# Kernel tuning notes

Hardware: AMD Instinct MI355X
Metric: run time of the kernel (lower is better)

Reference implementation:

```python
import jax, jax.numpy as jnp
import numpy as np

D_MODEL, D_LOW, NUM_BINS = 512, 64, 39
DIST_MIN, DIST_MAX = 2.0, 22.0
BIN_WIDTH = (DIST_MAX - DIST_MIN) / (NUM_BINS - 1)
LN_EPS = 1e-5


def setup_inputs() -> dict:
    key = jax.random.key(0)
    ks = jax.random.split(key, 10)
    B, N = 2, 768
    h_res = jax.random.normal(ks[0], (B, N, D_MODEL), dtype=jnp.float32)
    # scale coords so pairwise distances span the [2, 22] bin range
    x_true = jax.random.normal(ks[1], (B, N, 3), dtype=jnp.float32) * 5.0
    token_pad_mask = jnp.ones((B, N), dtype=jnp.float32)
    s = 1.0 / np.sqrt(D_MODEL)
    return {
        "h_res": h_res,
        "x_true": x_true,
        "token_pad_mask": token_pad_mask,
        "ln_w": jnp.ones((D_MODEL,), jnp.float32),
        "ln_b": jnp.zeros((D_MODEL,), jnp.float32),
        "wu_w": jax.random.normal(ks[2], (D_LOW, D_MODEL), jnp.float32) * s,
        "wu_b": jnp.zeros((D_LOW,), jnp.float32),
        "wv_w": jax.random.normal(ks[3], (D_LOW, D_MODEL), jnp.float32) * s,
        "wv_b": jnp.zeros((D_LOW,), jnp.float32),
        "wb_w": jax.random.normal(ks[4], (NUM_BINS, D_LOW), jnp.float32) * (1.0 / np.sqrt(D_LOW)),
        "wb_b": jnp.zeros((NUM_BINS,), jnp.float32),
    }


def _layernorm(x, w, b):
    mu = jnp.mean(x, axis=-1, keepdims=True)
    var = jnp.mean(jnp.square(x - mu), axis=-1, keepdims=True)
    return (x - mu) * jax.lax.rsqrt(var + LN_EPS) * w + b


def reference(h_res, x_true, token_pad_mask, ln_w, ln_b, wu_w, wu_b, wv_w, wv_b, wb_w, wb_b):
    B, N, _ = h_res.shape
    # pairwise distances -> target bins (trunc-to-int then clamp, as torch .long())
    diff = x_true[:, :, None, :] - x_true[:, None, :, :]          # [B,N,N,3]
    d_true = jnp.sqrt(jnp.sum(diff * diff, axis=-1))               # [B,N,N]
    target = jnp.clip(((d_true - DIST_MIN) / BIN_WIDTH).astype(jnp.int32), 0, NUM_BINS - 1)

    h = _layernorm(h_res, ln_w, ln_b)
    U = h @ wu_w.T + wu_b                                          # [B,N,d_low]
    V = h @ wv_w.T + wv_b                                          # [B,N,d_low]
    # logits[b,i,j,k] = sum_c U[b,i,c] V[b,j,c] Wb[k,c] + bb[k]
    logits = jnp.einsum("bic,bjc,kc->bijk", U, V, wb_w) + wb_b     # [B,N,N,K]
    logp = jax.nn.log_softmax(logits, axis=-1)
    ce = -jnp.take_along_axis(logp, target[..., None], axis=-1)[..., 0]  # [B,N,N]

    mask = (token_pad_mask[:, :, None] * token_pad_mask[:, None, :]) > 0  # [B,N,N] bool
    counts = jnp.sum(mask, axis=(1, 2))                            # [B]
    per_sample = jnp.sum(jnp.where(mask, ce, 0.0), axis=(1, 2)) / jnp.maximum(counts, 1)
    valid = counts > 0
    total_count = jnp.sum(valid)
    loss = jnp.sum(jnp.where(valid, per_sample, 0.0)) / jnp.maximum(total_count, 1)
    return loss
```

## Files before the change

kernel.cpp:

```cpp
#include <hip/hip_runtime.h>
#include <hip/hip_bf16.h>
#include <math.h>

#define D_MODEL 512
#define D_LOW   64
#define NBINS   39
#define LOG2E   1.4426950408889634f
#define LN2     0.6931471805599453f

typedef __attribute__((ext_vector_type(8))) short short8;
typedef __attribute__((ext_vector_type(4))) float floatx4;

__global__ __launch_bounds__(256) void prep_kernel(
    const float* __restrict__ ln_w, const float* __restrict__ ln_b,
    const float* __restrict__ wu_w, const float* __restrict__ wu_b,
    const float* __restrict__ wv_w, const float* __restrict__ wv_b,
    __hip_bfloat16* __restrict__ w2bf, float* __restrict__ w2sum,
    float* __restrict__ b2) {
  __shared__ float red[8];
  const int tid = threadIdx.x;
  const int o = blockIdx.x;
  const bool isU = (o < 64);
  const float* wrow = isU ? (wu_w + o * D_MODEL) : (wv_w + (o - 64) * D_MODEL);
  const float scale = isU ? LOG2E : 1.0f;

  float s1 = 0.f, s2 = 0.f;
  #pragma unroll
  for (int cc = 0; cc < 2; ++cc) {
    const int c = tid + cc * 256;
    const float w  = wrow[c];
    const float w2 = w * ln_w[c] * scale;
    const __hip_bfloat16 hb = __float2bfloat16(w2);
    w2bf[o * D_MODEL + c] = hb;
    s1 += __bfloat162float(hb);
    s2 += w * ln_b[c];
  }
  #pragma unroll
  for (int off = 32; off; off >>= 1) {
    s1 += __shfl_xor(s1, off);
    s2 += __shfl_xor(s2, off);
  }
  const int wave = tid >> 6, lane = tid & 63;
  if (lane == 0) { red[wave] = s1; red[4 + wave] = s2; }
  __syncthreads();
  if (tid == 0) {
    w2sum[o] = red[0] + red[1] + red[2] + red[3];
    const float ss2 = red[4] + red[5] + red[6] + red[7];
    b2[o] = scale * ((isU ? wu_b[o] : wv_b[o - 64]) + ss2);
  }
}

__global__ __launch_bounds__(512) void lnproj_kernel(
    const float* __restrict__ h_res, const __hip_bfloat16* __restrict__ w2bf,
    const float* __restrict__ w2sum, const float* __restrict__ b2,
    float* __restrict__ U, __hip_bfloat16* __restrict__ Vbf, int N) {
  __shared__ short abuf[16 * 512];
  __shared__ float sred[8][2][16];
  const int tid = threadIdx.x;
  const int wv = tid >> 6, lane = tid & 63;
  const int q = lane >> 4, ln16 = lane & 15;
  const int row0 = blockIdx.x * 16;

  float sum = 0.f, ssq = 0.f;
  #pragma unroll
  for (int k2 = 0; k2 < 2; ++k2) {
    const int kc = wv * 2 + k2;
    const float* hp = h_res + (size_t)(row0 + ln16) * D_MODEL + kc * 32 + q * 8;
    const floatx4 x0 = *reinterpret_cast<const floatx4*>(hp);
    const floatx4 x1 = *reinterpret_cast<const floatx4*>(hp + 4);
    short8 a;
    #pragma unroll
    for (int e = 0; e < 4; ++e) {
      sum += x0[e]; ssq += x0[e] * x0[e];
      const __hip_bfloat16 hb = __float2bfloat16(x0[e]);
      a[e] = *reinterpret_cast<const short*>(&hb);
    }
    #pragma unroll
    for (int e = 0; e < 4; ++e) {
      sum += x1[e]; ssq += x1[e] * x1[e];
      const __hip_bfloat16 hb = __float2bfloat16(x1[e]);
      a[4 + e] = *reinterpret_cast<const short*>(&hb);
    }
    *reinterpret_cast<short8*>(&abuf[kc * 512 + q * 128 + ln16 * 8]) = a;
  }
  sum += __shfl_xor(sum, 16); sum += __shfl_xor(sum, 32);
  ssq += __shfl_xor(ssq, 16); ssq += __shfl_xor(ssq, 32);
  if (lane < 16) { sred[wv][0][ln16] = sum; sred[wv][1][ln16] = ssq; }
  __syncthreads();

  float mu_r[4], rs_r[4];
  #pragma unroll
  for (int r = 0; r < 4; ++r) {
    const int row = q * 4 + r;
    float s = 0.f, s2 = 0.f;
    #pragma unroll
    for (int w = 0; w < 8; ++w) { s += sred[w][0][row]; s2 += sred[w][1][row]; }
    const float mu  = s * (1.0f / (float)D_MODEL);
    const float var = s2 * (1.0f / (float)D_MODEL) - mu * mu;
    mu_r[r] = mu;
    rs_r[r] = rsqrtf(var + 1e-5f);
  }

  const int out = wv * 16 + ln16;
  const short* wp = reinterpret_cast<const short*>(w2bf);
  floatx4 acc = (floatx4){0.f, 0.f, 0.f, 0.f};
  #pragma unroll
  for (int kc = 0; kc < 16; ++kc) {
    const short8 afr = *reinterpret_cast<const short8*>(
        &abuf[kc * 512 + q * 128 + ln16 * 8]);
    const short8 bfr = *reinterpret_cast<const short8*>(
        wp + (size_t)out * D_MODEL + kc * 32 + q * 8);
    acc = __builtin_amdgcn_mfma_f32_16x16x32_bf16(afr, bfr, acc, 0, 0, 0);
  }

  const float ws = w2sum[out];
  const float bb = b2[out];
  #pragma unroll
  for (int r = 0; r < 4; ++r) {
    const int rowg = row0 + q * 4 + r;
    const float val = rs_r[r] * acc[r] - mu_r[r] * rs_r[r] * ws + bb;
    if (out < 64) {
      U[(size_t)rowg * D_LOW + out] = val;
    } else {
      Vbf[(size_t)rowg * D_LOW + (out - 64)] = __float2bfloat16(val);
    }
  }
}

__global__ __launch_bounds__(256) void pair_kernel(
    const float* __restrict__ U, const __hip_bfloat16* __restrict__ Vbf,
    const float* __restrict__ wb_w, const float* __restrict__ wb_b,
    const float* __restrict__ x_true, const float* __restrict__ pmask,
    float* __restrict__ part, int N) {
  __shared__ short wsh[6 * 64 * 8];
  __shared__ float rbuf[8];
  const int i    = blockIdx.x;
  const int b    = blockIdx.y >> 1;
  const int half = blockIdx.y & 1;
  const int tid  = threadIdx.x;
  const int wave = tid >> 6, lane = tid & 63;
  const int q = lane >> 4, ln16 = lane & 15;
  const int rowi = b * N + i;
  const int jbase = half * (N >> 1) + wave * (N >> 3);
  const int q4 = q * 4;

  const short* Vp = reinterpret_cast<const short*>(Vbf) + (size_t)b * N * D_LOW;
  short8 v[6][2];
  #pragma unroll
  for (int tl = 0; tl < 6; ++tl) {
    const size_t jr = jbase + tl * 16 + ln16;
    v[tl][0] = *reinterpret_cast<const short8*>(Vp + jr * D_LOW + q * 8);
    v[tl][1] = *reinterpret_cast<const short8*>(Vp + jr * D_LOW + 32 + q * 8);
  }

  for (int slot = tid; slot < 384; slot += 256) {
    const int fidx = slot >> 6, l = slot & 63;
    const int t = fidx >> 1, s = fidx & 1;
    const int lq = l >> 4, l16 = l & 15;
    const int n = t * 16 + l16;
    short8 fr = (short8){0, 0, 0, 0, 0, 0, 0, 0};
    if (n < NBINS) {
      const float* up = U + (size_t)rowi * D_LOW + s * 32 + lq * 8;
      const float* wr = wb_w + (size_t)n * D_LOW + s * 32 + lq * 8;
      const floatx4 u0 = *reinterpret_cast<const floatx4*>(up);
      const floatx4 u1 = *reinterpret_cast<const floatx4*>(up + 4);
      const floatx4 w0 = *reinterpret_cast<const floatx4*>(wr);
      const floatx4 w1 = *reinterpret_cast<const floatx4*>(wr + 4);
      #pragma unroll
      for (int e = 0; e < 4; ++e) {
        const __hip_bfloat16 h0 = __float2bfloat16(u0[e] * w0[e]);
        const __hip_bfloat16 h1 = __float2bfloat16(u1[e] * w1[e]);
        fr[e]     = *reinterpret_cast<const short*>(&h0);
        fr[4 + e] = *reinterpret_cast<const short*>(&h1);
      }
    }
    *reinterpret_cast<short8*>(&wsh[slot * 8]) = fr;
  }

  const float xi0 = x_true[rowi * 3 + 0];
  const float xi1 = x_true[rowi * 3 + 1];
  const float xi2 = x_true[rowi * 3 + 2];
  const float pmi = pmask[rowi];
  const float BW  = (22.0f - 2.0f) / 38.0f;
  int tbv[6];
  #pragma unroll
  for (int tl = 0; tl < 6; ++tl) {
    const int rowj = b * N + jbase + tl * 16 + ln16;
    const float dx = xi0 - x_true[rowj * 3 + 0];
    const float dy = xi1 - x_true[rowj * 3 + 1];
    const float dz = xi2 - x_true[rowj * 3 + 2];
    const float d  = sqrtf(dx * dx + dy * dy + dz * dz);
    int tb = (int)((d - 2.0f) / BW);
    tb = tb < 0 ? 0 : (tb > NBINS - 1 ? NBINS - 1 : tb);
    tbv[tl] = (pmi * pmask[rowj] > 0.f) ? tb : -1;
  }

  floatx4 bias_init[3];
  #pragma unroll
  for (int t = 0; t < 3; ++t)
    #pragma unroll
    for (int r = 0; r < 4; ++r) {
      const int bin = t * 16 + q * 4 + r;
      bias_init[t][r] = (bin < NBINS) ? LOG2E * wb_b[bin] : -INFINITY;
    }

  __syncthreads();
  short8 wfrag[3][2];
  #pragma unroll
  for (int t = 0; t < 3; ++t)
    #pragma unroll
    for (int s = 0; s < 2; ++s)
      wfrag[t][s] = *reinterpret_cast<const short8*>(
          &wsh[((t * 2 + s) * 64 + lane) * 8]);

  float ce_sum = 0.f, cnt_sum = 0.f;
  #pragma unroll
  for (int tl = 0; tl < 6; ++tl) {
    floatx4 f[3];
    #pragma unroll
    for (int t = 0; t < 3; ++t) {
      floatx4 a = bias_init[t];
      a = __builtin_amdgcn_mfma_f32_16x16x32_bf16(wfrag[t][0], v[tl][0], a, 0, 0, 0);
      a = __builtin_amdgcn_mfma_f32_16x16x32_bf16(wfrag[t][1], v[tl][1], a, 0, 0, 0);
      f[t] = a;
    }

    const int tb  = tbv[tl];
    const int tbq = tb - q4;
    float s0 = 0.f, s1 = 0.f, s2 = 0.f, s3 = 0.f, lt = 0.f;
    #pragma unroll
    for (int t = 0; t < 3; ++t) {
      const floatx4 fv = f[t];
      s0 += __builtin_amdgcn_exp2f(fv[0]);
      s1 += __builtin_amdgcn_exp2f(fv[1]);
      s2 += __builtin_amdgcn_exp2f(fv[2]);
      s3 += __builtin_amdgcn_exp2f(fv[3]);
      lt += (tbq == t * 16 + 0) ? fv[0] : 0.f;
      lt += (tbq == t * 16 + 1) ? fv[1] : 0.f;
      lt += (tbq == t * 16 + 2) ? fv[2] : 0.f;
      lt += (tbq == t * 16 + 3) ? fv[3] : 0.f;
    }
    float ssum = (s0 + s1) + (s2 + s3);
    ssum += __shfl_xor(ssum, 16); ssum += __shfl_xor(ssum, 32);
    const float ok = (tb >= 0) ? 1.f : 0.f;
    ce_sum  += ok * LN2 * (__builtin_amdgcn_logf(ssum) - 4.0f * lt);
    cnt_sum += ok;
  }

  #pragma unroll
  for (int off = 32; off; off >>= 1) {
    ce_sum  += __shfl_xor(ce_sum, off);
    cnt_sum += __shfl_xor(cnt_sum, off);
  }
  if (lane == 0) { rbuf[wave] = ce_sum; rbuf[4 + wave] = cnt_sum; }
  __syncthreads();
  if (tid == 0) {
    const size_t slot = ((size_t)blockIdx.y * N + blockIdx.x) * 2;
    part[slot + 0] = rbuf[0] + rbuf[1] + rbuf[2] + rbuf[3];
    part[slot + 1] = rbuf[4] + rbuf[5] + rbuf[6] + rbuf[7];
  }
}

__global__ __launch_bounds__(256) void finalize_kernel(
    const float* __restrict__ part, float* __restrict__ out, int N, int B) {
  __shared__ float red[8];
  const int tid = threadIdx.x, wave = tid >> 6, lane = tid & 63;
  float loss = 0.f, vcount = 0.f;
  const int nper = 2 * N;
  for (int b = 0; b < B; ++b) {
    float ce = 0.f, cnt = 0.f;
    for (int e = tid; e < nper; e += 256) {
      const size_t base = ((size_t)b * nper + e) * 2;
      ce  += part[base + 0];
      cnt += part[base + 1];
    }
    #pragma unroll
    for (int off = 32; off; off >>= 1) {
      ce  += __shfl_xor(ce, off);
      cnt += __shfl_xor(cnt, off);
    }
    if (lane == 0) { red[wave] = ce; red[4 + wave] = cnt; }
    __syncthreads();
    if (tid == 0) {
      const float s = red[0] + red[1] + red[2] + red[3];
      const float c = red[4] + red[5] + red[6] + red[7];
      if (c > 0.f) { loss += s / fmaxf(c, 1.f); vcount += 1.f; }
    }
    __syncthreads();
  }
  if (tid == 0) out[0] = (vcount > 0.f) ? loss / vcount : 0.f;
}

extern "C" void kernel_launch(void* const* d_in, const int* in_sizes, int n_in,
                              void* d_out, int out_size, void* d_ws, size_t ws_size,
                              hipStream_t stream) {
  const float* h_res  = (const float*)d_in[0];
  const float* x_true = (const float*)d_in[1];
  const float* pmask  = (const float*)d_in[2];
  const float* ln_w   = (const float*)d_in[3];
  const float* ln_b   = (const float*)d_in[4];
  const float* wu_w   = (const float*)d_in[5];
  const float* wu_b   = (const float*)d_in[6];
  const float* wv_w   = (const float*)d_in[7];
  const float* wv_b   = (const float*)d_in[8];
  const float* wb_w   = (const float*)d_in[9];
  const float* wb_b   = (const float*)d_in[10];

  const int B  = 2;
  const int N  = in_sizes[2] / B;
  const int BN = B * N;

  float* U = (float*)d_ws;
  __hip_bfloat16* Vbf = (__hip_bfloat16*)(U + (size_t)BN * D_LOW);
  float* part = (float*)(Vbf + (size_t)BN * D_LOW);
  __hip_bfloat16* w2bf = (__hip_bfloat16*)(part + (size_t)2 * B * N * 2);
  float* w2sum = (float*)(w2bf + 128 * D_MODEL);
  float* b2    = w2sum + 128;

  prep_kernel<<<128, 256, 0, stream>>>(ln_w, ln_b, wu_w, wu_b, wv_w, wv_b,
                                       w2bf, w2sum, b2);
  lnproj_kernel<<<BN / 16, 512, 0, stream>>>(h_res, w2bf, w2sum, b2,
                                             U, Vbf, N);
  pair_kernel<<<dim3(N, 2 * B), 256, 0, stream>>>(
      U, Vbf, wb_w, wb_b, x_true, pmask, part, N);
  finalize_kernel<<<1, 256, 0, stream>>>(part, (float*)d_out, N, B);
}
```

Before: 124.5 us.

## Fuse weight prep into LN-projection and split pair work into quarters

Removes the separate prep kernel by having each projection block fold ln_w/ln_b into its own weight fragments, held in registers, and split the U/V outputs across a second grid dimension. The pair kernel now splits each row's j-range into four chunks instead of two, doubling the block count, and adds a launch-bounds occupancy hint. Its inner loop is restructured to issue all MFMAs first and then batch the softmax reductions and shuffles. The cost is redundant weight preprocessing in every projection block and doubled h_res reads and partial outputs.

```diff
diff --git a/kernel.cpp b/kernel.cpp
--- a/kernel.cpp
+++ b/kernel.cpp
@@ -11,60 +11,24 @@
 typedef __attribute__((ext_vector_type(8))) short short8;
 typedef __attribute__((ext_vector_type(4))) float floatx4;
 
-__global__ __launch_bounds__(256) void prep_kernel(
+__global__ __launch_bounds__(256) void lnp_kernel(
+    const float* __restrict__ h_res,
     const float* __restrict__ ln_w, const float* __restrict__ ln_b,
     const float* __restrict__ wu_w, const float* __restrict__ wu_b,
     const float* __restrict__ wv_w, const float* __restrict__ wv_b,
-    __hip_bfloat16* __restrict__ w2bf, float* __restrict__ w2sum,
-    float* __restrict__ b2) {
-  __shared__ float red[8];
-  const int tid = threadIdx.x;
-  const int o = blockIdx.x;
-  const bool isU = (o < 64);
-  const float* wrow = isU ? (wu_w + o * D_MODEL) : (wv_w + (o - 64) * D_MODEL);
-  const float scale = isU ? LOG2E : 1.0f;
-
-  float s1 = 0.f, s2 = 0.f;
-  #pragma unroll
-  for (int cc = 0; cc < 2; ++cc) {
-    const int c = tid + cc * 256;
-    const float w  = wrow[c];
-    const float w2 = w * ln_w[c] * scale;
-    const __hip_bfloat16 hb = __float2bfloat16(w2);
-    w2bf[o * D_MODEL + c] = hb;
-    s1 += __bfloat162float(hb);
-    s2 += w * ln_b[c];
-  }
-  #pragma unroll
-  for (int off = 32; off; off >>= 1) {
-    s1 += __shfl_xor(s1, off);
-    s2 += __shfl_xor(s2, off);
-  }
-  const int wave = tid >> 6, lane = tid & 63;
-  if (lane == 0) { red[wave] = s1; red[4 + wave] = s2; }
-  __syncthreads();
-  if (tid == 0) {
-    w2sum[o] = red[0] + red[1] + red[2] + red[3];
-    const float ss2 = red[4] + red[5] + red[6] + red[7];
-    b2[o] = scale * ((isU ? wu_b[o] : wv_b[o - 64]) + ss2);
-  }
-}
-
-__global__ __launch_bounds__(512) void lnproj_kernel(
-    const float* __restrict__ h_res, const __hip_bfloat16* __restrict__ w2bf,
-    const float* __restrict__ w2sum, const float* __restrict__ b2,
     float* __restrict__ U, __hip_bfloat16* __restrict__ Vbf, int N) {
   __shared__ short abuf[16 * 512];
-  __shared__ float sred[8][2][16];
+  __shared__ float sred[4][2][16];
   const int tid = threadIdx.x;
   const int wv = tid >> 6, lane = tid & 63;
   const int q = lane >> 4, ln16 = lane & 15;
   const int row0 = blockIdx.x * 16;
+  const int og = blockIdx.y;
 
   float sum = 0.f, ssq = 0.f;
   #pragma unroll
-  for (int k2 = 0; k2 < 2; ++k2) {
-    const int kc = wv * 2 + k2;
+  for (int k2 = 0; k2 < 4; ++k2) {
+    const int kc = wv * 4 + k2;
     const float* hp = h_res + (size_t)(row0 + ln16) * D_MODEL + kc * 32 + q * 8;
     const floatx4 x0 = *reinterpret_cast<const floatx4*>(hp);
     const floatx4 x1 = *reinterpret_cast<const floatx4*>(hp + 4);
@@ -86,6 +50,42 @@
   sum += __shfl_xor(sum, 16); sum += __shfl_xor(sum, 32);
   ssq += __shfl_xor(ssq, 16); ssq += __shfl_xor(ssq, 32);
   if (lane < 16) { sred[wv][0][ln16] = sum; sred[wv][1][ln16] = ssq; }
+
+  const int oloc = wv * 16 + ln16;
+  const float scale = og ? 1.0f : LOG2E;
+  const float* wrow = (og ? wv_w : wu_w) + (size_t)oloc * D_MODEL;
+  short8 bfrag[16];
+  float ws = 0.f, sb = 0.f;
+  #pragma unroll
+  for (int kc = 0; kc < 16; ++kc) {
+    const int c0 = kc * 32 + q * 8;
+    const floatx4 w0 = *reinterpret_cast<const floatx4*>(wrow + c0);
+    const floatx4 w1 = *reinterpret_cast<const floatx4*>(wrow + c0 + 4);
+    const floatx4 lw0 = *reinterpret_cast<const floatx4*>(ln_w + c0);
+    const floatx4 lw1 = *reinterpret_cast<const floatx4*>(ln_w + c0 + 4);
+    const floatx4 lb0 = *reinterpret_cast<const floatx4*>(ln_b + c0);
+    const floatx4 lb1 = *reinterpret_cast<const floatx4*>(ln_b + c0 + 4);
+    short8 f;
+    #pragma unroll
+    for (int e = 0; e < 4; ++e) {
+      const float t0 = w0[e] * lw0[e] * scale;
+      const __hip_bfloat16 h0 = __float2bfloat16(t0);
+      f[e] = *reinterpret_cast<const short*>(&h0);
+      ws += __bfloat162float(h0);
+      sb += w0[e] * lb0[e];
+
+      const float t1 = w1[e] * lw1[e] * scale;
+      const __hip_bfloat16 h1 = __float2bfloat16(t1);
+      f[4 + e] = *reinterpret_cast<const short*>(&h1);
+      ws += __bfloat162float(h1);
+      sb += w1[e] * lb1[e];
+    }
+    bfrag[kc] = f;
+  }
+  ws += __shfl_xor(ws, 16); ws += __shfl_xor(ws, 32);
+  sb += __shfl_xor(sb, 16); sb += __shfl_xor(sb, 32);
+  const float bb = scale * ((og ? wv_b[oloc] : wu_b[oloc]) + sb);
+
   __syncthreads();
 
   float mu_r[4], rs_r[4];
@@ -94,40 +94,34 @@
     const int row = q * 4 + r;
     float s = 0.f, s2 = 0.f;
     #pragma unroll
-    for (int w = 0; w < 8; ++w) { s += sred[w][0][row]; s2 += sred[w][1][row]; }
+    for (int w = 0; w < 4; ++w) { s += sred[w][0][row]; s2 += sred[w][1][row]; }
     const float mu  = s * (1.0f / (float)D_MODEL);
     const float var = s2 * (1.0f / (float)D_MODEL) - mu * mu;
     mu_r[r] = mu;
     rs_r[r] = rsqrtf(var + 1e-5f);
   }
 
-  const int out = wv * 16 + ln16;
-  const short* wp = reinterpret_cast<const short*>(w2bf);
   floatx4 acc = (floatx4){0.f, 0.f, 0.f, 0.f};
   #pragma unroll
   for (int kc = 0; kc < 16; ++kc) {
     const short8 afr = *reinterpret_cast<const short8*>(
         &abuf[kc * 512 + q * 128 + ln16 * 8]);
-    const short8 bfr = *reinterpret_cast<const short8*>(
-        wp + (size_t)out * D_MODEL + kc * 32 + q * 8);
-    acc = __builtin_amdgcn_mfma_f32_16x16x32_bf16(afr, bfr, acc, 0, 0, 0);
-  }
-
-  const float ws = w2sum[out];
-  const float bb = b2[out];
+    acc = __builtin_amdgcn_mfma_f32_16x16x32_bf16(afr, bfrag[kc], acc, 0, 0, 0);
+  }
+
   #pragma unroll
   for (int r = 0; r < 4; ++r) {
     const int rowg = row0 + q * 4 + r;
     const float val = rs_r[r] * acc[r] - mu_r[r] * rs_r[r] * ws + bb;
-    if (out < 64) {
-      U[(size_t)rowg * D_LOW + out] = val;
+    if (og == 0) {
+      U[(size_t)rowg * D_LOW + oloc] = val;
     } else {
-      Vbf[(size_t)rowg * D_LOW + (out - 64)] = __float2bfloat16(val);
+      Vbf[(size_t)rowg * D_LOW + oloc] = __float2bfloat16(val);
     }
   }
 }
 
-__global__ __launch_bounds__(256) void pair_kernel(
+__global__ __launch_bounds__(256, 4) void pair_kernel(
     const float* __restrict__ U, const __hip_bfloat16* __restrict__ Vbf,
     const float* __restrict__ wb_w, const float* __restrict__ wb_b,
     const float* __restrict__ x_true, const float* __restrict__ pmask,
@@ -135,19 +129,19 @@
   __shared__ short wsh[6 * 64 * 8];
   __shared__ float rbuf[8];
   const int i    = blockIdx.x;
-  const int b    = blockIdx.y >> 1;
-  const int half = blockIdx.y & 1;
+  const int b    = blockIdx.y >> 2;
+  const int qtr  = blockIdx.y & 3;
   const int tid  = threadIdx.x;
   const int wave = tid >> 6, lane = tid & 63;
   const int q = lane >> 4, ln16 = lane & 15;
   const int rowi = b * N + i;
-  const int jbase = half * (N >> 1) + wave * (N >> 3);
+  const int jbase = qtr * (N >> 2) + wave * (N >> 4);
   const int q4 = q * 4;
 
   const short* Vp = reinterpret_cast<const short*>(Vbf) + (size_t)b * N * D_LOW;
-  short8 v[6][2];
-  #pragma unroll
-  for (int tl = 0; tl < 6; ++tl) {
+  short8 v[3][2];
+  #pragma unroll
+  for (int tl = 0; tl < 3; ++tl) {
     const size_t jr = jbase + tl * 16 + ln16;
     v[tl][0] = *reinterpret_cast<const short8*>(Vp + jr * D_LOW + q * 8);
     v[tl][1] = *reinterpret_cast<const short8*>(Vp + jr * D_LOW + 32 + q * 8);
@@ -182,9 +176,9 @@
   const float xi2 = x_true[rowi * 3 + 2];
   const float pmi = pmask[rowi];
   const float BW  = (22.0f - 2.0f) / 38.0f;
-  int tbv[6];
-  #pragma unroll
-  for (int tl = 0; tl < 6; ++tl) {
+  int tbv[3];
+  #pragma unroll
+  for (int tl = 0; tl < 3; ++tl) {
     const int rowj = b * N + jbase + tl * 16 + ln16;
     const float dx = xi0 - x_true[rowj * 3 + 0];
     const float dy = xi1 - x_true[rowj * 3 + 1];
@@ -213,24 +207,25 @@
       wfrag[t][s] = *reinterpret_cast<const short8*>(
           &wsh[((t * 2 + s) * 64 + lane) * 8]);
 
-  float ce_sum = 0.f, cnt_sum = 0.f;
-  #pragma unroll
-  for (int tl = 0; tl < 6; ++tl) {
-    floatx4 f[3];
+  floatx4 f[3][3];
+  #pragma unroll
+  for (int tl = 0; tl < 3; ++tl)
     #pragma unroll
     for (int t = 0; t < 3; ++t) {
       floatx4 a = bias_init[t];
       a = __builtin_amdgcn_mfma_f32_16x16x32_bf16(wfrag[t][0], v[tl][0], a, 0, 0, 0);
       a = __builtin_amdgcn_mfma_f32_16x16x32_bf16(wfrag[t][1], v[tl][1], a, 0, 0, 0);
-      f[t] = a;
-    }
-
-    const int tb  = tbv[tl];
-    const int tbq = tb - q4;
+      f[tl][t] = a;
+    }
+
+  float sp[3], ltv[3];
+  #pragma unroll
+  for (int tl = 0; tl < 3; ++tl) {
+    const int tbq = tbv[tl] - q4;
     float s0 = 0.f, s1 = 0.f, s2 = 0.f, s3 = 0.f, lt = 0.f;
     #pragma unroll
     for (int t = 0; t < 3; ++t) {
-      const floatx4 fv = f[t];
+      const floatx4 fv = f[tl][t];
       s0 += __builtin_amdgcn_exp2f(fv[0]);
       s1 += __builtin_amdgcn_exp2f(fv[1]);
       s2 += __builtin_amdgcn_exp2f(fv[2]);
@@ -240,10 +235,20 @@
       lt += (tbq == t * 16 + 2) ? fv[2] : 0.f;
       lt += (tbq == t * 16 + 3) ? fv[3] : 0.f;
     }
-    float ssum = (s0 + s1) + (s2 + s3);
-    ssum += __shfl_xor(ssum, 16); ssum += __shfl_xor(ssum, 32);
-    const float ok = (tb >= 0) ? 1.f : 0.f;
-    ce_sum  += ok * LN2 * (__builtin_amdgcn_logf(ssum) - 4.0f * lt);
+    sp[tl] = (s0 + s1) + (s2 + s3);
+    ltv[tl] = lt;
+  }
+
+  #pragma unroll
+  for (int tl = 0; tl < 3; ++tl) sp[tl] += __shfl_xor(sp[tl], 16);
+  #pragma unroll
+  for (int tl = 0; tl < 3; ++tl) sp[tl] += __shfl_xor(sp[tl], 32);
+
+  float ce_sum = 0.f, cnt_sum = 0.f;
+  #pragma unroll
+  for (int tl = 0; tl < 3; ++tl) {
+    const float ok = (tbv[tl] >= 0) ? 1.f : 0.f;
+    ce_sum  += ok * LN2 * (__builtin_amdgcn_logf(sp[tl]) - 4.0f * ltv[tl]);
     cnt_sum += ok;
   }
 
@@ -266,7 +271,7 @@
   __shared__ float red[8];
   const int tid = threadIdx.x, wave = tid >> 6, lane = tid & 63;
   float loss = 0.f, vcount = 0.f;
-  const int nper = 2 * N;
+  const int nper = 4 * N;
   for (int b = 0; b < B; ++b) {
     float ce = 0.f, cnt = 0.f;
     for (int e = tid; e < nper; e += 256) {
@@ -313,15 +318,10 @@
   float* U = (float*)d_ws;
   __hip_bfloat16* Vbf = (__hip_bfloat16*)(U + (size_t)BN * D_LOW);
   float* part = (float*)(Vbf + (size_t)BN * D_LOW);
-  __hip_bfloat16* w2bf = (__hip_bfloat16*)(part + (size_t)2 * B * N * 2);
-  float* w2sum = (float*)(w2bf + 128 * D_MODEL);
-  float* b2    = w2sum + 128;
-
-  prep_kernel<<<128, 256, 0, stream>>>(ln_w, ln_b, wu_w, wu_b, wv_w, wv_b,
-                                       w2bf, w2sum, b2);
-  lnproj_kernel<<<BN / 16, 512, 0, stream>>>(h_res, w2bf, w2sum, b2,
-                                             U, Vbf, N);
-  pair_kernel<<<dim3(N, 2 * B), 256, 0, stream>>>(
+
+  lnp_kernel<<<dim3(BN / 16, 2), 256, 0, stream>>>(
+      h_res, ln_w, ln_b, wu_w, wu_b, wv_w, wv_b, U, Vbf, N);
+  pair_kernel<<<dim3(N, 4 * B), 256, 0, stream>>>(
       U, Vbf, wb_w, wb_b, x_true, pmask, part, N);
   finalize_kernel<<<1, 256, 0, stream>>>(part, (float*)d_out, N, B);
 }
```

Result: slower. 134.3 us (+7.8%).
